# Optimization experiments

Hardware: AMD Instinct MI355X
Metric: run time of the kernel (lower is better)

## Reference

```python
import jax, jax.numpy as jnp
import numpy as np

B = 2048          # number of trees (batch)
K = 511           # nodes per complete binary tree (depth 9: levels 0..8)
DEPTH = 9
VOCAB = 200000
EDIM = 128


def setup_inputs() -> dict:
    key = jax.random.key(0)
    k1, k2, k3, k4 = jax.random.split(key, 4)
    N = B * K
    i = np.arange(K)
    lvl = np.floor(np.log2(i + 1)).astype(np.int32)            # level within tree, 0..8
    par_local = np.where(i > 0, (i - 1) // 2, 0).astype(np.int64)  # root points to itself
    offs = (np.arange(B, dtype=np.int64) * K)[:, None]
    parent = jnp.asarray((offs + par_local[None, :]).reshape(-1), dtype=jnp.int32)
    level = jnp.asarray(np.tile(lvl, B), dtype=jnp.int32)
    batch_id = jnp.asarray(np.repeat(np.arange(B, dtype=np.int64), K), dtype=jnp.int32)
    tokens = jax.random.randint(k1, (N,), 0, VOCAB, dtype=jnp.int32)
    emb_weight = jax.random.normal(k2, (VOCAB, EDIM), dtype=jnp.float32) * 0.02
    W = jax.random.normal(k3, (EDIM, EDIM), dtype=jnp.float32) * 0.05
    b = jax.random.normal(k4, (EDIM,), dtype=jnp.float32) * 0.01
    return {"emb_weight": emb_weight, "W": W, "b": b,
            "tokens": tokens, "parent": parent, "level": level, "batch_id": batch_id}


def reference(emb_weight, W, b, tokens, parent, level, batch_id):
    # per-node projection: W_c(embedding(token))  -> [N, EDIM]
    h = emb_weight[tokens] @ W + b
    # bottom-up child aggregation: h[parent] += h[child], deepest level first
    for l in range(DEPTH - 1, 0, -1):
        contrib = jnp.where((level == l)[:, None], h, 0.0)
        h = h.at[parent].add(contrib)
    # torch.max over all node_list snapshots == per-tree elementwise max of node
    # states, clamped at 0 by the zero rows of untouched batch_node snapshots.
    seg_max = jax.ops.segment_max(h, batch_id, num_segments=B)
    return jnp.maximum(seg_max, 0.0)
```

## Files before the change

### kernel.cpp

```cpp
#include <hip/hip_runtime.h>
#include <hip/hip_bf16.h>
#include <stdint.h>

#define VOCAB 200000
#define EDIM 128
#define NTREES 2048
#define KNODES 511

typedef __attribute__((ext_vector_type(4))) float f32x4;
typedef __attribute__((ext_vector_type(2))) float f32x2;
typedef __attribute__((ext_vector_type(8))) short s16x8;
typedef __attribute__((ext_vector_type(8))) unsigned short u16x8;

__device__ __forceinline__ unsigned short f2bf(float x) {
  unsigned u = __builtin_bit_cast(unsigned, x);
  return (unsigned short)((u + 0x7fffu + ((u >> 16) & 1u)) >> 16);
}
__device__ __forceinline__ float bf2f(unsigned short h) {
  unsigned u = ((unsigned)h) << 16;
  return __builtin_bit_cast(float, u);
}

__device__ __forceinline__ unsigned fp8enc(float v) {
  unsigned u = __builtin_bit_cast(unsigned, v);
  unsigned s = (u >> 24) & 0x80u;
  unsigned au = u & 0x7fffffffu;
  au = au > 0x43E00000u ? 0x43E00000u : au;
  unsigned r = au + 0x0007ffffu + ((au >> 20) & 1u);
  unsigned code = (((r >> 23) - 120u) << 3) | ((r >> 20) & 7u);
  float a = __builtin_bit_cast(float, au);
  unsigned sub = (unsigned)(int)rintf(a * 512.0f);
  unsigned c = (au < 0x3C800000u) ? sub : code;
  return c | s;
}
__device__ __forceinline__ float fp8dec(unsigned b) {
  unsigned e = (b >> 3) & 15u, m = b & 7u;
  float n = __builtin_bit_cast(float, ((e + 120u) << 23) | (m << 20));
  float sv = (float)(int)m * 0.001953125f;
  float v = e ? n : sv;
  return (b & 0x80u) ? -v : v;
}

__device__ __forceinline__ unsigned enc4(float a, float b, float c, float d) {
#if __has_builtin(__builtin_amdgcn_cvt_pk_fp8_f32)
  int pk = 0;
  pk = __builtin_amdgcn_cvt_pk_fp8_f32(a, b, pk, false);
  pk = __builtin_amdgcn_cvt_pk_fp8_f32(c, d, pk, true);
  return (unsigned)pk;
#else
  return fp8enc(a) | (fp8enc(b) << 8) | (fp8enc(c) << 16) | (fp8enc(d) << 24);
#endif
}

__device__ __forceinline__ void dec8(uint2 v, float* o) {
#if __has_builtin(__builtin_amdgcn_cvt_pk_f32_fp8)
  f32x2 a = __builtin_amdgcn_cvt_pk_f32_fp8(v.x, false);
  f32x2 b = __builtin_amdgcn_cvt_pk_f32_fp8(v.x, true);
  f32x2 c = __builtin_amdgcn_cvt_pk_f32_fp8(v.y, false);
  f32x2 d = __builtin_amdgcn_cvt_pk_f32_fp8(v.y, true);
  o[0] = a[0]; o[1] = a[1]; o[2] = b[0]; o[3] = b[1];
  o[4] = c[0]; o[5] = c[1]; o[6] = d[0]; o[7] = d[1];
#else
#pragma unroll
  for (int i = 0; i < 4; ++i) o[i] = fp8dec((v.x >> (8 * i)) & 0xFFu);
#pragma unroll
  for (int i = 0; i < 4; ++i) o[4 + i] = fp8dec((v.y >> (8 * i)) & 0xFFu);
#endif
}

__device__ __forceinline__ s16x8 cvt8(f32x4 a, f32x4 b) {
  u16x8 t;
#pragma unroll
  for (int i = 0; i < 4; ++i)
    t[i] = __builtin_bit_cast(unsigned short, __float2bfloat16(a[i]));
#pragma unroll
  for (int i = 0; i < 4; ++i)
    t[4 + i] = __builtin_bit_cast(unsigned short, __float2bfloat16(b[i]));
  return __builtin_bit_cast(s16x8, t);
}

__global__ __launch_bounds__(256) void wprep_kernel(
    const float* __restrict__ W, const float* __restrict__ b,
    unsigned short* __restrict__ WTb2, float* __restrict__ bsc) {
  int c = blockIdx.x * 256 + threadIdx.x;
  if (c < 2048) {
    int lane = c & 63, fr = c >> 6;
    int ks = fr >> 3, nt = fr & 7, q = lane >> 4, cl = lane & 15;
    u16x8 t;
#pragma unroll
    for (int j = 0; j < 8; ++j)
      t[j] = f2bf(W[(ks * 32 + q * 8 + j) * EDIM + nt * 16 + cl] * 64.0f);
    *(u16x8*)(WTb2 + c * 8) = t;
  }
  if (c < EDIM) bsc[c] = b[c] * 64.0f;
}

__global__ __launch_bounds__(512, 2) void proj_kernel(
    const float* __restrict__ emb, const unsigned short* __restrict__ WTb2,
    const float* __restrict__ bsc, unsigned char* __restrict__ T8) {
  __shared__ float ES[8][16][EDIM];

  const int tid = threadIdx.x;
  const int wv = tid >> 6, lane = tid & 63;
  const int q = lane >> 4, cl = lane & 15;

  s16x8 wf[32];
#pragma unroll
  for (int fr = 0; fr < 32; ++fr)
    wf[fr] = *(const s16x8*)(WTb2 + (fr * 64 + lane) * 8);
  f32x4 bb[8];
#pragma unroll
  for (int nt = 0; nt < 8; ++nt)
    bb[nt] = *(const f32x4*)(bsc + nt * 16 + q * 4);
#pragma unroll
  for (int fr = 0; fr < 32; ++fr) asm volatile("" : "+v"(wf[fr]));
#pragma unroll
  for (int nt = 0; nt < 8; ++nt) asm volatile("" : "+v"(bb[nt]));

  const int gw = blockIdx.x * 8 + wv;
  const int NWT = VOCAB / 16;
  const int STRIDE = 256 * 8;

  auto issue_dma = [&](int t) {
#pragma unroll
    for (int i = 0; i < 8; ++i) {
      int rloc = 2 * i + (lane >> 5);
      int c5 = lane & 31;
      int csrc = (c5 & 24) | ((c5 & 7) ^ (rloc & 7));
      const float* src = emb + ((long)t * 16 + rloc) * EDIM + csrc * 4;
      __builtin_amdgcn_global_load_lds(
          (const __attribute__((address_space(1))) unsigned int*)src,
          (__attribute__((address_space(3))) unsigned int*)(&ES[wv][2 * i][0]),
          16, 0, 0);
    }
  };

  int t = gw;
  issue_dma(t);
  for (; t < NWT; t += STRIDE) {
    const int tn = t + STRIDE;

    asm volatile("s_waitcnt vmcnt(0)" ::: "memory");
    __builtin_amdgcn_sched_barrier(0);

    f32x4 ea[4], eb[4];
#pragma unroll
    for (int ks = 0; ks < 4; ++ks) {
      int g0 = ks * 8 + q * 2;
      int s0 = (g0 & 24) | ((g0 & 7) ^ (cl & 7));
      int g1 = g0 + 1;
      int s1 = (g1 & 24) | ((g1 & 7) ^ (cl & 7));
      const float* rb = &ES[wv][cl][0];
      ea[ks] = *(const f32x4*)(rb + s0 * 4);
      eb[ks] = *(const f32x4*)(rb + s1 * 4);
    }
    asm volatile("s_waitcnt lgkmcnt(0)" ::: "memory");
    __builtin_amdgcn_sched_barrier(0);
    if (tn < NWT) issue_dma(tn);

    f32x4 acc[8];
#pragma unroll
    for (int nt = 0; nt < 8; ++nt) acc[nt] = bb[nt];
#pragma unroll
    for (int ks = 0; ks < 4; ++ks) {
      s16x8 ef = cvt8(ea[ks], eb[ks]);
#pragma unroll
      for (int nt = 0; nt < 8; ++nt)
        acc[nt] = __builtin_amdgcn_mfma_f32_16x16x32_bf16(wf[ks * 8 + nt], ef, acc[nt], 0, 0, 0);
    }

    const long row = (long)t * 16 + cl;
#pragma unroll
    for (int nt = 0; nt < 8; ++nt) {
      const int col0 = nt * 16 + q * 4;
      *(unsigned*)&T8[row * EDIM + col0] =
          enc4(acc[nt][0], acc[nt][1], acc[nt][2], acc[nt][3]);
    }
  }
}

__global__ __launch_bounds__(512, 4) void tree_kernel(
    const unsigned char* __restrict__ T8, const int* __restrict__ tokens,
    float* __restrict__ out) {
  __shared__ unsigned char P8[512][EDIM];
  unsigned char* lds = &P8[0][0];
  const int SOFF = 16384;
  const int MOFF = 53248;

  const int tid = threadIdx.x;
  const int tree = blockIdx.x;
  const int wv = tid >> 6, lane = tid & 63;

  const int* tk = tokens + (long)tree * KNODES;
  int toks[8];
#pragma unroll
  for (int i = 0; i < 8; ++i) {
    int node = wv * 64 + i * 8 + (lane >> 3);
    toks[i] = tk[node > 510 ? 510 : node];
  }
  const int chunk = (lane & 7) ^ ((lane >> 3) & 7);
#pragma unroll
  for (int i = 0; i < 8; ++i) {
    const unsigned char* src = T8 + (long)toks[i] * EDIM + chunk * 16;
    unsigned char* dst = &P8[wv * 64 + i * 8][0];
    __builtin_amdgcn_global_load_lds(
        (const __attribute__((address_space(1))) unsigned int*)src,
        (__attribute__((address_space(3))) unsigned int*)dst, 16, 0, 0);
  }
  __syncthreads();

  auto ldP8 = [&](int row, int q8) -> uint2 {
    int g = q8 >> 1, h = q8 & 1;
    return *(const uint2*)(lds + row * 128 + (((g ^ (row & 7))) << 4) + h * 8);
  };
  auto saddr = [&](int slot, int q16) -> unsigned char* {
    return lds + SOFF + slot * 288 + ((q16 ^ (slot & 7)) << 4);
  };

  const int q = tid & 15;
  const int jg = tid >> 4;
  float rmax[8];
#pragma unroll
  for (int e = 0; e < 8; ++e) rmax[e] = 0.f;

  u16x8 sp7[4];
#pragma unroll
  for (int k = 0; k < 4; ++k) {
    const int p = jg + 32 * k, m = 127 + p;
    uint2 pr = ldP8(m, q);
    uint2 xr = ldP8(2 * m + 1, q);
    uint2 yr = ldP8(2 * m + 2, q);
    float pv[8], xv[8], yv[8];
    dec8(pr, pv); dec8(xr, xv); dec8(yr, yv);
#pragma unroll
    for (int e = 0; e < 8; ++e) {
      float sv = pv[e] + xv[e] + yv[e];
      rmax[e] = fmaxf(rmax[e], fmaxf(fmaxf(xv[e], yv[e]), sv));
      sp7[k][e] = f2bf(sv);
    }
  }
  __syncthreads();
#pragma unroll
  for (int k = 0; k < 4; ++k) *(u16x8*)saddr(jg + 32 * k, q) = sp7[k];
  __syncthreads();

  for (int l = 6; l >= 0; --l) {
    const int cnt = 1 << l;
    for (int p = jg; p < cnt; p += 32) {
      const int m = cnt - 1 + p;
      const int ps = p << (7 - l);
      const int c2s = ps + (1 << (6 - l));
      uint2 pr = ldP8(m, q);
      u16x8 c1 = *(const u16x8*)saddr(ps, q);
      u16x8 c2 = *(const u16x8*)saddr(c2s, q);
      float pv[8];
      dec8(pr, pv);
      u16x8 sp;
#pragma unroll
      for (int e = 0; e < 8; ++e) {
        float sv = pv[e] + bf2f(c1[e]) + bf2f(c2[e]);
        rmax[e] = fmaxf(rmax[e], sv);
        sp[e] = f2bf(sv);
      }
      *(u16x8*)saddr(ps, q) = sp;
    }
    __syncthreads();
  }

#pragma unroll
  for (int e = 0; e < 8; ++e) {
    rmax[e] = fmaxf(rmax[e], __shfl_xor(rmax[e], 16, 64));
    rmax[e] = fmaxf(rmax[e], __shfl_xor(rmax[e], 32, 64));
  }
  float* mb = (float*)(lds + MOFF);
  if (lane < 16) {
#pragma unroll
    for (int e = 0; e < 8; ++e) mb[wv * 128 + lane * 8 + e] = rmax[e];
  }
  __syncthreads();
  if (tid < 128) {
    float v = mb[tid];
#pragma unroll
    for (int w2 = 1; w2 < 8; ++w2) v = fmaxf(v, mb[w2 * 128 + tid]);
    out[(long)tree * 128 + tid] = v * 0.015625f;
  }
}

extern "C" void kernel_launch(void* const* d_in, const int* in_sizes, int n_in,
                              void* d_out, int out_size, void* d_ws, size_t ws_size,
                              hipStream_t stream) {
  const float* emb = (const float*)d_in[0];
  const float* W = (const float*)d_in[1];
  const float* b = (const float*)d_in[2];
  const int* tokens = (const int*)d_in[3];

  unsigned char* T8 = (unsigned char*)d_ws;
  unsigned short* WTb2 = (unsigned short*)((char*)d_ws + 25600000);
  float* bsc = (float*)((char*)d_ws + 25632768);
  float* out = (float*)d_out;

  wprep_kernel<<<8, 256, 0, stream>>>(W, b, WTb2, bsc);
  proj_kernel<<<256, 512, 0, stream>>>(emb, WTb2, bsc, T8);
  tree_kernel<<<NTREES, 512, 0, stream>>>(T8, tokens, out);
}
```

Baseline: 66.38 us.

## Double-buffer embedding DMA in projection and stage fp8 output through LDS

The projection kernel now keeps two LDS buffers per wave, so the embedding tile two iterations ahead is already in flight while the current one is computed. Partial vmcnt waits replace the full drain. The fp8 results are first written to a padded LDS staging tile and then stored to global memory as coalesced 16-byte rows instead of scattered 4-byte writes. The launch shape changes to 512 blocks of 256 threads. The extra LDS and the hand-counted vmcnt values add occupancy and correctness risk.

```diff
diff --git a/kernel.cpp b/kernel.cpp
--- a/kernel.cpp
+++ b/kernel.cpp
@@ -6,11 +6,16 @@
 #define EDIM 128
 #define NTREES 2048
 #define KNODES 511
+#define PROJ_GRID 512
 
 typedef __attribute__((ext_vector_type(4))) float f32x4;
 typedef __attribute__((ext_vector_type(2))) float f32x2;
 typedef __attribute__((ext_vector_type(8))) short s16x8;
 typedef __attribute__((ext_vector_type(8))) unsigned short u16x8;
+typedef __attribute__((ext_vector_type(4))) unsigned int u32x4;
+
+#define AS1 __attribute__((address_space(1)))
+#define AS3 __attribute__((address_space(3)))
 
 __device__ __forceinline__ unsigned short f2bf(float x) {
   unsigned u = __builtin_bit_cast(unsigned, x);
@@ -95,10 +100,11 @@
   if (c < EDIM) bsc[c] = b[c] * 64.0f;
 }
 
-__global__ __launch_bounds__(512, 2) void proj_kernel(
+__global__ __launch_bounds__(256) void proj_kernel(
     const float* __restrict__ emb, const unsigned short* __restrict__ WTb2,
     const float* __restrict__ bsc, unsigned char* __restrict__ T8) {
-  __shared__ float ES[8][16][EDIM];
+  __shared__ char DB[4][2][8192];
+  __shared__ char ST[4][16 * 144];
 
   const int tid = threadIdx.x;
   const int wv = tid >> 6, lane = tid & 63;
@@ -117,11 +123,11 @@
 #pragma unroll
   for (int nt = 0; nt < 8; ++nt) asm volatile("" : "+v"(bb[nt]));
 
-  const int gw = blockIdx.x * 8 + wv;
-  const int NWT = VOCAB / 16;
-  const int STRIDE = 256 * 8;
-
-  auto issue_dma = [&](int t) {
+  const int NT = VOCAB / 16;
+  const int NW = PROJ_GRID * 4;
+  const int gw = blockIdx.x * 4 + wv;
+
+  auto issue_dma = [&](int buf, int t) {
 #pragma unroll
     for (int i = 0; i < 8; ++i) {
       int rloc = 2 * i + (lane >> 5);
@@ -129,20 +135,28 @@
       int csrc = (c5 & 24) | ((c5 & 7) ^ (rloc & 7));
       const float* src = emb + ((long)t * 16 + rloc) * EDIM + csrc * 4;
       __builtin_amdgcn_global_load_lds(
-          (const __attribute__((address_space(1))) unsigned int*)src,
-          (__attribute__((address_space(3))) unsigned int*)(&ES[wv][2 * i][0]),
-          16, 0, 0);
+          (const AS1 unsigned int*)src,
+          (AS3 unsigned int*)(&DB[wv][buf][i * 1024]), 16, 0, 0);
     }
   };
 
-  int t = gw;
-  issue_dma(t);
-  for (; t < NWT; t += STRIDE) {
-    const int tn = t + STRIDE;
-
-    asm volatile("s_waitcnt vmcnt(0)" ::: "memory");
+  issue_dma(0, gw);
+  issue_dma(1, gw + NW);
+
+  int k = 0;
+  for (int t = gw; t < NT; t += NW, ++k) {
+    const int buf = k & 1;
+
+    if (k == 0) {
+      asm volatile("s_waitcnt vmcnt(8)" ::: "memory");
+    } else if (t + NW < NT) {
+      asm volatile("s_waitcnt vmcnt(12)" ::: "memory");
+    } else {
+      asm volatile("s_waitcnt vmcnt(4)" ::: "memory");
+    }
     __builtin_amdgcn_sched_barrier(0);
 
+    const char* rb = &DB[wv][buf][cl * 512];
     f32x4 ea[4], eb[4];
 #pragma unroll
     for (int ks = 0; ks < 4; ++ks) {
@@ -150,13 +164,14 @@
       int s0 = (g0 & 24) | ((g0 & 7) ^ (cl & 7));
       int g1 = g0 + 1;
       int s1 = (g1 & 24) | ((g1 & 7) ^ (cl & 7));
-      const float* rb = &ES[wv][cl][0];
-      ea[ks] = *(const f32x4*)(rb + s0 * 4);
-      eb[ks] = *(const f32x4*)(rb + s1 * 4);
+      ea[ks] = *(const f32x4*)(rb + s0 * 16);
+      eb[ks] = *(const f32x4*)(rb + s1 * 16);
     }
     asm volatile("s_waitcnt lgkmcnt(0)" ::: "memory");
     __builtin_amdgcn_sched_barrier(0);
-    if (tn < NWT) issue_dma(tn);
+
+    const int n2 = t + 2 * NW;
+    if (n2 < NT) issue_dma(buf, n2);
 
     f32x4 acc[8];
 #pragma unroll
@@ -169,12 +184,22 @@
         acc[nt] = __builtin_amdgcn_mfma_f32_16x16x32_bf16(wf[ks * 8 + nt], ef, acc[nt], 0, 0, 0);
     }
 
-    const long row = (long)t * 16 + cl;
+    char* sw = &ST[wv][0] + cl * 144;
 #pragma unroll
     for (int nt = 0; nt < 8; ++nt) {
-      const int col0 = nt * 16 + q * 4;
-      *(unsigned*)&T8[row * EDIM + col0] =
-          enc4(acc[nt][0], acc[nt][1], acc[nt][2], acc[nt][3]);
+      unsigned pk = enc4(acc[nt][0], acc[nt][1], acc[nt][2], acc[nt][3]);
+      *(unsigned*)(sw + (nt * 4 + q) * 4) = pk;
+    }
+    asm volatile("s_waitcnt lgkmcnt(0)" ::: "memory");
+    __builtin_amdgcn_sched_barrier(0);
+
+    const long tb8 = (long)t * 16 * EDIM;
+#pragma unroll
+    for (int j = 0; j < 2; ++j) {
+      const int slot = j * 64 + lane;
+      const int r = slot >> 3, c16 = slot & 7;
+      u32x4 v = *(const u32x4*)(&ST[wv][0] + r * 144 + c16 * 16);
+      *(u32x4*)&T8[tb8 + slot * 16] = v;
     }
   }
 }
@@ -203,9 +228,8 @@
   for (int i = 0; i < 8; ++i) {
     const unsigned char* src = T8 + (long)toks[i] * EDIM + chunk * 16;
     unsigned char* dst = &P8[wv * 64 + i * 8][0];
-    __builtin_amdgcn_global_load_lds(
-        (const __attribute__((address_space(1))) unsigned int*)src,
-        (__attribute__((address_space(3))) unsigned int*)dst, 16, 0, 0);
+    __builtin_amdgcn_global_load_lds((const AS1 unsigned int*)src,
+                                     (AS3 unsigned int*)dst, 16, 0, 0);
   }
   __syncthreads();
 
@@ -300,6 +324,6 @@
   float* out = (float*)d_out;
 
   wprep_kernel<<<8, 256, 0, stream>>>(W, b, WTb2, bsc);
-  proj_kernel<<<256, 512, 0, stream>>>(emb, WTb2, bsc, T8);
+  proj_kernel<<<PROJ_GRID, 256, 0, stream>>>(emb, WTb2, bsc, T8);
   tree_kernel<<<NTREES, 512, 0, stream>>>(T8, tokens, out);
 }
```

New measurement: 65.61 us. Within noise of the previous version (-1.1%).
